# Optimization experiments

Measured on AMD Instinct MI355X. Metric: run time of the kernel, lower is better.

Reference implementation:

```python
import jax, jax.numpy as jnp
import numpy as np

B, S, D = 4, 2048, 2048
E = 8            # num_experts
TOP_K = 2
H = 1408         # intermediate_size per expert
SH = 2 * H       # shared expert intermediate (shared_experts=2)


def setup_inputs() -> dict:
    key = jax.random.key(0)
    ks = jax.random.split(key, 8)
    sc = 0.02
    return {
        "hidden_states": jax.random.normal(ks[0], (B, S, D), jnp.float32),
        "gate_w": jax.random.normal(ks[1], (E, D), jnp.float32) * sc,   # torch Linear weight [out,in]
        "w1": jax.random.normal(ks[2], (E, H, D), jnp.float32) * sc,    # gate_proj per expert
        "w3": jax.random.normal(ks[3], (E, H, D), jnp.float32) * sc,    # up_proj per expert
        "w2": jax.random.normal(ks[4], (E, D, H), jnp.float32) * sc,    # down_proj per expert
        "sw1": jax.random.normal(ks[5], (SH, D), jnp.float32) * sc,
        "sw3": jax.random.normal(ks[6], (SH, D), jnp.float32) * sc,
        "sw2": jax.random.normal(ks[7], (D, SH), jnp.float32) * sc,
    }


def reference(hidden_states, gate_w, w1, w3, w2, sw1, sw3, sw2):
    b, s, d = hidden_states.shape
    x = hidden_states.reshape(-1, d)                      # [T, D]
    logits = x @ gate_w.T                                 # [T, E]
    rw, sel = jax.lax.top_k(logits, TOP_K)                # [T, K]
    rw = jax.nn.softmax(rw, axis=-1)                      # norm_topk_prob=True
    onehot = jax.nn.one_hot(sel, E, dtype=x.dtype)        # [T, K, E]
    token_mask = onehot.sum(axis=1)                       # [T, E] in {0,1}
    # NOTE: faithful to the source quirk: expert_weights.sum(dim=-1) on a flat
    # masked gather sums routing weights over ALL tokens selecting the expert,
    # producing one scalar per expert.
    s_e = (rw[..., None] * onehot).sum(axis=(0, 1))       # [E]
    combine = token_mask * s_e                            # [T, E]
    # per-expert SwiGLU MLP on all tokens (dense combine form of gather/scatter)
    g = jnp.einsum('td,ehd->eth', x, w1)                  # [E, T, H]
    u = jnp.einsum('td,ehd->eth', x, w3)
    a = jax.nn.silu(g) * u
    y = jnp.einsum('eth,edh->etd', a, w2)                 # [E, T, D]
    out = jnp.einsum('te,etd->td', combine, y)            # [T, D]
    shared = (jax.nn.silu(x @ sw1.T) * (x @ sw3.T)) @ sw2.T
    out = out + shared
    return out.reshape(b, s, d)
```

## Files before the change

kernel.cpp:

```cpp
#include <hip/hip_runtime.h>
#include <hip/hip_bf16.h>
#include <stdint.h>

#define T_TOK 8192
#define DIM   2048
#define NEXP  8
#define HDIM  1408
#define SHDIM 2816

typedef __attribute__((ext_vector_type(8))) short bfrag;
typedef __attribute__((ext_vector_type(4))) float f32x4;
typedef __attribute__((ext_vector_type(4))) short s16x4;

__device__ __forceinline__ short f2bf(float f) {
    union { float f; uint32_t u; } v; v.f = f;
    return (short)((v.u + 0x8000u) >> 16);
}
__device__ __forceinline__ float bf2f(short s) {
    union { uint32_t u; float f; } v; v.u = ((uint32_t)(uint16_t)s) << 16;
    return v.f;
}

__device__ __forceinline__ bfrag cvt8(float4 a, float4 b) {
    bfrag r;
    r[0] = f2bf(a.x); r[1] = f2bf(a.y); r[2] = f2bf(a.z); r[3] = f2bf(a.w);
    r[4] = f2bf(b.x); r[5] = f2bf(b.y); r[6] = f2bf(b.z); r[7] = f2bf(b.w);
    return r;
}

__device__ __forceinline__ void gload16(const void* g, void* l) {
    __builtin_amdgcn_global_load_lds(
        (__attribute__((address_space(1))) void*)(g),
        (__attribute__((address_space(3))) void*)(l), 16, 0, 0);
}

#define MFMA16(a, b, c) __builtin_amdgcn_mfma_f32_16x16x32_bf16((a), (b), (c), 0, 0, 0)


__global__ __launch_bounds__(256) void gate_kernel(
    const float* __restrict__ x, const float* __restrict__ gw,
    __hip_bfloat16* __restrict__ xbf,
    int* __restrict__ sel, int* __restrict__ meta, float* __restrict__ s_e)
{
    __shared__ float g[NEXP * DIM];
    for (int i = threadIdx.x; i < NEXP * DIM; i += 256) g[i] = gw[i];
    __syncthreads();
    const int wid = threadIdx.x >> 6, lane = threadIdx.x & 63;
    for (int it = 0; it < 8; ++it) {
        const int t = blockIdx.x * 32 + wid * 8 + it;
        float acc[NEXP];
#pragma unroll
        for (int e = 0; e < NEXP; ++e) acc[e] = 0.f;
        const float4* xr = (const float4*)(x + (size_t)t * DIM);
        for (int j = 0; j < DIM / 4; j += 64) {
            float4 xv = xr[j + lane];
            s16x4 xv16 = { f2bf(xv.x), f2bf(xv.y), f2bf(xv.z), f2bf(xv.w) };
            *(s16x4*)&xbf[(size_t)t * DIM + (j + lane) * 4] = xv16;
#pragma unroll
            for (int e = 0; e < NEXP; ++e) {
                float4 gv = *(const float4*)&g[e * DIM + (j + lane) * 4];
                acc[e] += xv.x * gv.x + xv.y * gv.y + xv.z * gv.z + xv.w * gv.w;
            }
        }
#pragma unroll
        for (int e = 0; e < NEXP; ++e)
            for (int o = 32; o; o >>= 1) acc[e] += __shfl_xor(acc[e], o);
        if (lane == 0) {
            int e0 = 0; float v0 = acc[0];
#pragma unroll
            for (int e = 1; e < NEXP; ++e) if (acc[e] > v0) { v0 = acc[e]; e0 = e; }
            int e1 = -1; float v1 = -3.4e38f;
#pragma unroll
            for (int e = 0; e < NEXP; ++e) if (e != e0 && acc[e] > v1) { v1 = acc[e]; e1 = e; }
            float p0 = 1.f / (1.f + __expf(v1 - v0));
            float p1 = 1.f - p0;
            sel[2 * t] = e0; sel[2 * t + 1] = e1;
            atomicAdd(&s_e[e0], p0); atomicAdd(&s_e[e1], p1);
            atomicAdd(&meta[e0], 1); atomicAdd(&meta[e1], 1);
        }
    }
}

__global__ void scan_kernel(int* meta) {
    if (threadIdx.x == 0) {
        int acc = 0;
        for (int e = 0; e < NEXP; ++e) {
            meta[16 + e] = acc;
            meta[8 + e]  = acc;
            acc += meta[e];
        }
        meta[24] = acc;
    }
}

__global__ __launch_bounds__(256) void fill_kernel(
    const int* __restrict__ sel, int* __restrict__ meta,
    int* __restrict__ list, int2* __restrict__ slots)
{
    const int t = blockIdx.x * 256 + threadIdx.x;
    int e0 = sel[2 * t], e1 = sel[2 * t + 1];
    int p0 = atomicAdd(&meta[8 + e0], 1); list[p0] = t;
    int p1 = atomicAdd(&meta[8 + e1], 1); list[p1] = t;
    slots[t] = make_int2(p0, p1);
}

#define C1 2883584
#define C2 5767168
#define C3 8650752
#define C4 9371648
#define C5 10092544
#define C6 10813440
__global__ __launch_bounds__(256) void cvt6_kernel(
    const float* __restrict__ s0, const float* __restrict__ s1, const float* __restrict__ s2,
    const float* __restrict__ s3, const float* __restrict__ s4, const float* __restrict__ s5,
    __hip_bfloat16* __restrict__ d0, __hip_bfloat16* __restrict__ d1, __hip_bfloat16* __restrict__ d2,
    __hip_bfloat16* __restrict__ d3, __hip_bfloat16* __restrict__ d4, __hip_bfloat16* __restrict__ d5)
{
    const int stride = gridDim.x * 256;
    for (int i = blockIdx.x * 256 + threadIdx.x; i < C6; i += stride) {
        const float* s; __hip_bfloat16* d; int off;
        if      (i < C1) { s = s0; d = d0; off = i; }
        else if (i < C2) { s = s1; d = d1; off = i - C1; }
        else if (i < C3) { s = s2; d = d2; off = i - C2; }
        else if (i < C4) { s = s3; d = d3; off = i - C3; }
        else if (i < C5) { s = s4; d = d4; off = i - C4; }
        else             { s = s5; d = d5; off = i - C5; }
        const float4* p = (const float4*)(s + (size_t)off * 8);
        float4 a = p[0], b = p[1];
        *(bfrag*)(d + (size_t)off * 8) = cvt8(a, b);
    }
}


template<int N, bool GATHER>
__global__ __launch_bounds__(512, 2) void up_v6(
    const __hip_bfloat16* __restrict__ X,
    const __hip_bfloat16* __restrict__ W1,
    const __hip_bfloat16* __restrict__ W3,
    __hip_bfloat16* __restrict__ act,
    const int* __restrict__ list,
    const int* __restrict__ meta)
{
    constexpr int K = DIM;
    constexpr int NP = K / 32;
    constexpr int nx = N / 128, ny = T_TOK / 256, nz = GATHER ? NEXP : 1;
    constexpr int nwg = nx * ny * nz, cpx = nwg / 8;
    const int bid = (int)blockIdx.x + nx * ((int)blockIdx.y + ny * (int)blockIdx.z);
    const int virt = (bid & 7) * cpx + (bid >> 3);
    const int xi = virt % nx;
    const int rest = virt / nx;
    const int yi = rest % ny;
    const int e = rest / ny;

    int count, base;
    if (GATHER) {
        count = meta[e]; base = meta[16 + e];
        if (yi * 256 >= count) return;
    } else { count = T_TOK; base = 0; }
    const int m0 = yi * 256, n0 = xi * 128;

    __shared__ alignas(16) short As[4][256 * 32];
    __shared__ alignas(16) short B1s[4][128 * 32];
    __shared__ alignas(16) short B3s[4][128 * 32];

    const int tid = threadIdx.x, wid = tid >> 6, lane = tid & 63;

    const int u    = (tid & 7) ^ ((tid >> 3) & 7);
    const int srow = 2 * (tid >> 3) + (u >> 2);
    const int sslot = u & 3;

    const __hip_bfloat16* pA[2];
#pragma unroll
    for (int q = 0; q < 2; ++q) {
        int r = m0 + srow + q * 128; if (r > count - 1) r = count - 1;
        int ga = GATHER ? list[base + r] : r;
        pA[q] = X + (size_t)ga * K + sslot * 8;
    }
    const __hip_bfloat16* pB1 = W1 + ((size_t)e * N + n0 + srow) * K + sslot * 8;
    const __hip_bfloat16* pB3 = W3 + ((size_t)e * N + n0 + srow) * K + sslot * 8;

#define STAGE_UP(H, BUF) do { const int k0_ = (H) * 32;                         \
    gload16(pA[0] + k0_, &As[BUF][tid * 8]);                                    \
    gload16(pA[1] + k0_, &As[BUF][4096 + tid * 8]);                             \
    gload16(pB1   + k0_, &B1s[BUF][tid * 8]);                                   \
    gload16(pB3   + k0_, &B3s[BUF][tid * 8]); } while (0)

    const int wm = wid >> 2, wn = wid & 3;
    const int l15 = lane & 15, lhi = lane >> 4;
    const int vswz = (((lhi + 4 * (l15 & 1)) ^ (l15 >> 1)) << 4);
    const int arb  = (l15 >> 1) * 128 + vswz;

    f32x4 accg[8][2], accu[8][2];
#pragma unroll
    for (int i = 0; i < 8; ++i)
#pragma unroll
        for (int j = 0; j < 2; ++j) { accg[i][j] = 0.f; accu[i][j] = 0.f; }

    STAGE_UP(0, 0);
    STAGE_UP(1, 1);
    STAGE_UP(2, 2);

#pragma unroll 4
    for (int p = 0; p < NP; ++p) {
        const int cur = p & 3;
        asm volatile("s_waitcnt vmcnt(8)" ::: "memory");
        __builtin_amdgcn_s_barrier();
        __builtin_amdgcn_sched_barrier(0);
        const int ps = (p + 3 < NP) ? (p + 3) : (NP - 1);
        STAGE_UP(ps, (p + 3) & 3);
        __builtin_amdgcn_sched_barrier(0);
        bfrag b1f[2], b3f[2];
#pragma unroll
        for (int j = 0; j < 2; ++j) {
            const int off = wn * 2048 + j * 1024 + arb;
            b1f[j] = *(const bfrag*)((const char*)B1s[cur] + off);
            b3f[j] = *(const bfrag*)((const char*)B3s[cur] + off);
        }
        __builtin_amdgcn_s_setprio(1);
#pragma unroll
        for (int i = 0; i < 8; ++i) {
            bfrag a = *(const bfrag*)((const char*)As[cur] + wm * 8192 + i * 1024 + arb);
#pragma unroll
            for (int j = 0; j < 2; ++j) {
                accg[i][j] = MFMA16(a, b1f[j], accg[i][j]);
                accu[i][j] = MFMA16(a, b3f[j], accu[i][j]);
            }
        }
        __builtin_amdgcn_s_setprio(0);
    }
#undef STAGE_UP
    asm volatile("s_waitcnt vmcnt(0)" ::: "memory");

#pragma unroll
    for (int i = 0; i < 8; ++i)
#pragma unroll
        for (int r = 0; r < 4; ++r) {
            int m = wm * 128 + i * 16 + lhi * 4 + r;
            if (m0 + m < count) {
#pragma unroll
                for (int j = 0; j < 2; ++j) {
                    float gg = accg[i][j][r];
                    float uu = accu[i][j][r];
                    float a = gg / (1.f + __expf(-gg)) * uu;
                    int n = n0 + wn * 32 + j * 16 + l15;
                    act[(size_t)(base + m0 + m) * N + n] = __float2bfloat16(a);
                }
            }
        }
}

template<int KD, bool TO_BF16>
__global__ __launch_bounds__(512, 2) void down_v6(
    const __hip_bfloat16* __restrict__ A,
    const __hip_bfloat16* __restrict__ W2,
    float* __restrict__ out,
    __hip_bfloat16* __restrict__ yscr,
    const int* __restrict__ meta)
{
    constexpr int N = DIM;
    constexpr int NP = KD / 32;
    constexpr int nx = N / 256, ny = T_TOK / 256, nz = TO_BF16 ? NEXP : 1;
    constexpr int nwg = nx * ny * nz, cpx = nwg / 8;
    const int bid = (int)blockIdx.x + nx * ((int)blockIdx.y + ny * (int)blockIdx.z);
    const int virt = (bid & 7) * cpx + (bid >> 3);
    const int xi = virt % nx;
    const int rest = virt / nx;
    const int yi = rest % ny;
    const int e = rest / ny;

    int count, base;
    if (TO_BF16) {
        count = meta[e]; base = meta[16 + e];
        if (yi * 256 >= count) return;
    } else { count = T_TOK; base = 0; }
    const int m0 = yi * 256, n0 = xi * 256;

    __shared__ alignas(16) short As[4][256 * 32];
    __shared__ alignas(16) short Bs[4][256 * 32];

    const int tid = threadIdx.x, wid = tid >> 6, lane = tid & 63;

    const int u    = (tid & 7) ^ ((tid >> 3) & 7);
    const int srow = 2 * (tid >> 3) + (u >> 2);
    const int sslot = u & 3;

    const __hip_bfloat16* pA[2];
    const __hip_bfloat16* pB[2];
#pragma unroll
    for (int q = 0; q < 2; ++q) {
        int r = m0 + srow + q * 128; if (r > count - 1) r = count - 1;
        pA[q] = A  + (size_t)(base + r) * KD + sslot * 8;
        pB[q] = W2 + ((size_t)e * N + n0 + srow + q * 128) * KD + sslot * 8;
    }

#define STAGE_DN(H, BUF) do { const int k0_ = (H) * 32;                         \
    gload16(pA[0] + k0_, &As[BUF][tid * 8]);                                    \
    gload16(pA[1] + k0_, &As[BUF][4096 + tid * 8]);                             \
    gload16(pB[0] + k0_, &Bs[BUF][tid * 8]);                                    \
    gload16(pB[1] + k0_, &Bs[BUF][4096 + tid * 8]); } while (0)

    const int wm = wid >> 2, wn = wid & 3;
    const int l15 = lane & 15, lhi = lane >> 4;
    const int vswz = (((lhi + 4 * (l15 & 1)) ^ (l15 >> 1)) << 4);
    const int arb  = (l15 >> 1) * 128 + vswz;

    f32x4 acc[8][4];
#pragma unroll
    for (int i = 0; i < 8; ++i)
#pragma unroll
        for (int j = 0; j < 4; ++j) acc[i][j] = 0.f;

    STAGE_DN(0, 0);
    STAGE_DN(1, 1);
    STAGE_DN(2, 2);

#pragma unroll 4
    for (int p = 0; p < NP; ++p) {
        const int cur = p & 3;
        asm volatile("s_waitcnt vmcnt(8)" ::: "memory");
        __builtin_amdgcn_s_barrier();
        __builtin_amdgcn_sched_barrier(0);
        const int ps = (p + 3 < NP) ? (p + 3) : (NP - 1);
        STAGE_DN(ps, (p + 3) & 3);
        __builtin_amdgcn_sched_barrier(0);
        bfrag bf[4];
#pragma unroll
        for (int j = 0; j < 4; ++j)
            bf[j] = *(const bfrag*)((const char*)Bs[cur] + wn * 4096 + j * 1024 + arb);
        __builtin_amdgcn_s_setprio(1);
#pragma unroll
        for (int i = 0; i < 8; ++i) {
            bfrag a = *(const bfrag*)((const char*)As[cur] + wm * 8192 + i * 1024 + arb);
#pragma unroll
            for (int j = 0; j < 4; ++j)
                acc[i][j] = MFMA16(a, bf[j], acc[i][j]);
        }
        __builtin_amdgcn_s_setprio(0);
    }
#undef STAGE_DN
    asm volatile("s_waitcnt vmcnt(0)" ::: "memory");

#pragma unroll
    for (int i = 0; i < 8; ++i)
#pragma unroll
        for (int r = 0; r < 4; ++r) {
            int m = wm * 128 + i * 16 + lhi * 4 + r;
            if (m0 + m < count) {
#pragma unroll
                for (int j = 0; j < 4; ++j) {
                    int n = n0 + wn * 64 + j * 16 + l15;
                    if (TO_BF16)
                        yscr[(size_t)(base + m0 + m) * DIM + n] = __float2bfloat16(acc[i][j][r]);
                    else
                        out[(size_t)(m0 + m) * DIM + n] = acc[i][j][r];
                }
            }
        }
}

__global__ __launch_bounds__(256) void combine_kernel(
    float* __restrict__ out, const __hip_bfloat16* __restrict__ yscr,
    const int* __restrict__ sel, const int2* __restrict__ slots,
    const float* __restrict__ s_e)
{
    const int t = blockIdx.x;
    const int d = threadIdx.x * 8;
    const int2 sl = slots[t];
    const float se0 = s_e[sel[2 * t]];
    const float se1 = s_e[sel[2 * t + 1]];
    bfrag y0 = *(const bfrag*)&yscr[(size_t)sl.x * DIM + d];
    bfrag y1 = *(const bfrag*)&yscr[(size_t)sl.y * DIM + d];
    float4* o = (float4*)(out + (size_t)t * DIM + d);
    float4 o0 = o[0], o1 = o[1];
    o0.x += se0 * bf2f(y0[0]) + se1 * bf2f(y1[0]);
    o0.y += se0 * bf2f(y0[1]) + se1 * bf2f(y1[1]);
    o0.z += se0 * bf2f(y0[2]) + se1 * bf2f(y1[2]);
    o0.w += se0 * bf2f(y0[3]) + se1 * bf2f(y1[3]);
    o1.x += se0 * bf2f(y0[4]) + se1 * bf2f(y1[4]);
    o1.y += se0 * bf2f(y0[5]) + se1 * bf2f(y1[5]);
    o1.z += se0 * bf2f(y0[6]) + se1 * bf2f(y1[6]);
    o1.w += se0 * bf2f(y0[7]) + se1 * bf2f(y1[7]);
    o[0] = o0; o[1] = o1;
}

extern "C" void kernel_launch(void* const* d_in, const int* in_sizes, int n_in,
                              void* d_out, int out_size, void* d_ws, size_t ws_size,
                              hipStream_t stream) {
    const float* x   = (const float*)d_in[0];
    const float* gw  = (const float*)d_in[1];
    const float* w1  = (const float*)d_in[2];
    const float* w3  = (const float*)d_in[3];
    const float* w2  = (const float*)d_in[4];
    const float* sw1 = (const float*)d_in[5];
    const float* sw3 = (const float*)d_in[6];
    const float* sw2 = (const float*)d_in[7];
    float* out = (float*)d_out;

    const size_t SZ_X   = (size_t)T_TOK * DIM * 2;
    const size_t SZ_W   = (size_t)NEXP * HDIM * DIM * 2;
    const size_t SZ_SW  = (size_t)SHDIM * DIM * 2;
    const size_t SZ_ACT = (size_t)2 * T_TOK * HDIM * 2;
    const size_t need = SZ_X + 3 * SZ_W + 3 * SZ_SW + SZ_ACT
                      + (size_t)4 * T_TOK * sizeof(int)
                      + (size_t)2 * T_TOK * sizeof(int)  + 512;
    if (need > ws_size) return;

    char* p = (char*)d_ws;
    __hip_bfloat16* xbf   = (__hip_bfloat16*)p; p += SZ_X;
    __hip_bfloat16* w1bf  = (__hip_bfloat16*)p; p += SZ_W;
    __hip_bfloat16* w3bf  = (__hip_bfloat16*)p; p += SZ_W;
    __hip_bfloat16* w2bf  = (__hip_bfloat16*)p; p += SZ_W;
    __hip_bfloat16* sw1bf = (__hip_bfloat16*)p; p += SZ_SW;
    __hip_bfloat16* sw3bf = (__hip_bfloat16*)p; p += SZ_SW;
    __hip_bfloat16* sw2bf = (__hip_bfloat16*)p; p += SZ_SW;
    __hip_bfloat16* act   = (__hip_bfloat16*)p; p += SZ_ACT;
    int*  list  = (int*)p;  p += (size_t)2 * T_TOK * sizeof(int);
    int*  sel   = (int*)p;  p += (size_t)2 * T_TOK * sizeof(int);
    int2* slots = (int2*)p; p += (size_t)2 * T_TOK * sizeof(int);
    int*  meta  = (int*)p;
    float* s_e  = (float*)(meta + 32);
    __hip_bfloat16* yscr = (__hip_bfloat16*)d_ws;

    hipMemsetAsync(meta, 0, 256, stream);
    gate_kernel<<<T_TOK / 32, 256, 0, stream>>>(x, gw, xbf, sel, meta, s_e);
    scan_kernel<<<1, 64, 0, stream>>>(meta);
    fill_kernel<<<T_TOK / 256, 256, 0, stream>>>(sel, meta, list, slots);

    cvt6_kernel<<<2048, 256, 0, stream>>>(w1, w3, w2, sw1, sw3, sw2,
                                          w1bf, w3bf, w2bf, sw1bf, sw3bf, sw2bf);

    up_v6<SHDIM, false><<<dim3(SHDIM / 128, T_TOK / 256, 1), 512, 0, stream>>>(
        xbf, sw1bf, sw3bf, act, nullptr, meta);
    down_v6<SHDIM, false><<<dim3(DIM / 256, T_TOK / 256, 1), 512, 0, stream>>>(
        act, sw2bf, out, nullptr, meta);
    up_v6<HDIM, true><<<dim3(HDIM / 128, T_TOK / 256, NEXP), 512, 0, stream>>>(
        xbf, w1bf, w3bf, act, list, meta);
    down_v6<HDIM, true><<<dim3(DIM / 256, T_TOK / 256, NEXP), 512, 0, stream>>>(
        act, w2bf, out, yscr, meta);
    combine_kernel<<<T_TOK, 256, 0, stream>>>(out, yscr, sel, slots, s_e);
}
```

Baseline: 1.118 ms.

## Split GEMM k-step into two barrier-separated phases interleaving loads with MFMA

Each k-iteration of the up and down GEMM kernels is split into two halves. The A-tile global-to-LDS loads are issued before the first half of the MFMAs and the B-tile loads before the second half. Fragment reads are hoisted ahead of explicit lgkmcnt fences and workgroup barriers, in a ping-pong style schedule. The aim is to spread memory issue across the MFMA work and keep the waves in lockstep, at the cost of four extra barriers per iteration.

```diff
diff --git a/kernel.cpp b/kernel.cpp
--- a/kernel.cpp
+++ b/kernel.cpp
@@ -35,6 +35,8 @@
 }
 
 #define MFMA16(a, b, c) __builtin_amdgcn_mfma_f32_16x16x32_bf16((a), (b), (c), 0, 0, 0)
+#define LGKM0_FENCE() do { asm volatile("s_waitcnt lgkmcnt(0)" ::: "memory"); \
+                           __builtin_amdgcn_sched_barrier(0); } while (0)
 
 
 __global__ __launch_bounds__(256) void gate_kernel(
@@ -133,7 +135,7 @@
 
 
 template<int N, bool GATHER>
-__global__ __launch_bounds__(512, 2) void up_v6(
+__global__ __launch_bounds__(512, 2) void up_v7(
     const __hip_bfloat16* __restrict__ X,
     const __hip_bfloat16* __restrict__ W1,
     const __hip_bfloat16* __restrict__ W3,
@@ -179,56 +181,84 @@
     const __hip_bfloat16* pB1 = W1 + ((size_t)e * N + n0 + srow) * K + sslot * 8;
     const __hip_bfloat16* pB3 = W3 + ((size_t)e * N + n0 + srow) * K + sslot * 8;
 
-#define STAGE_UP(H, BUF) do { const int k0_ = (H) * 32;                         \
+    const int wm = wid >> 2, wn = wid & 3;
+    const int l15 = lane & 15, lhi = lane >> 4;
+    const int vswz = (((lhi + 4 * (l15 & 1)) ^ (l15 >> 1)) << 4);
+    const int arb  = (l15 >> 1) * 128 + vswz;
+
+    f32x4 accg[8][2], accu[8][2];
+#pragma unroll
+    for (int i = 0; i < 8; ++i)
+#pragma unroll
+        for (int j = 0; j < 2; ++j) { accg[i][j] = 0.f; accu[i][j] = 0.f; }
+
+#define STAGE_ALL(H, BUF) do { const int k0_ = (H) * 32;                        \
     gload16(pA[0] + k0_, &As[BUF][tid * 8]);                                    \
     gload16(pA[1] + k0_, &As[BUF][4096 + tid * 8]);                             \
     gload16(pB1   + k0_, &B1s[BUF][tid * 8]);                                   \
     gload16(pB3   + k0_, &B3s[BUF][tid * 8]); } while (0)
-
-    const int wm = wid >> 2, wn = wid & 3;
-    const int l15 = lane & 15, lhi = lane >> 4;
-    const int vswz = (((lhi + 4 * (l15 & 1)) ^ (l15 >> 1)) << 4);
-    const int arb  = (l15 >> 1) * 128 + vswz;
-
-    f32x4 accg[8][2], accu[8][2];
-#pragma unroll
-    for (int i = 0; i < 8; ++i)
-#pragma unroll
-        for (int j = 0; j < 2; ++j) { accg[i][j] = 0.f; accu[i][j] = 0.f; }
-
-    STAGE_UP(0, 0);
-    STAGE_UP(1, 1);
-    STAGE_UP(2, 2);
+    STAGE_ALL(0, 0);
+    STAGE_ALL(1, 1);
+    STAGE_ALL(2, 2);
+#undef STAGE_ALL
 
 #pragma unroll 4
     for (int p = 0; p < NP; ++p) {
         const int cur = p & 3;
+        const int ps = (p + 3 < NP) ? (p + 3) : (NP - 1);
+        const int pb = (p + 3) & 3;
+        const int k0s = ps * 32;
+
         asm volatile("s_waitcnt vmcnt(8)" ::: "memory");
         __builtin_amdgcn_s_barrier();
         __builtin_amdgcn_sched_barrier(0);
-        const int ps = (p + 3 < NP) ? (p + 3) : (NP - 1);
-        STAGE_UP(ps, (p + 3) & 3);
-        __builtin_amdgcn_sched_barrier(0);
-        bfrag b1f[2], b3f[2];
+        gload16(pA[0] + k0s, &As[pb][tid * 8]);
+        gload16(pA[1] + k0s, &As[pb][4096 + tid * 8]);
+        __builtin_amdgcn_sched_barrier(0);
+        bfrag b1f[2], b3f[2], af[4];
 #pragma unroll
         for (int j = 0; j < 2; ++j) {
             const int off = wn * 2048 + j * 1024 + arb;
             b1f[j] = *(const bfrag*)((const char*)B1s[cur] + off);
             b3f[j] = *(const bfrag*)((const char*)B3s[cur] + off);
         }
+#pragma unroll
+        for (int i = 0; i < 4; ++i)
+            af[i] = *(const bfrag*)((const char*)As[cur] + wm * 8192 + i * 1024 + arb);
+        __builtin_amdgcn_s_barrier();
+        LGKM0_FENCE();
         __builtin_amdgcn_s_setprio(1);
 #pragma unroll
-        for (int i = 0; i < 8; ++i) {
-            bfrag a = *(const bfrag*)((const char*)As[cur] + wm * 8192 + i * 1024 + arb);
+        for (int i = 0; i < 4; ++i)
 #pragma unroll
             for (int j = 0; j < 2; ++j) {
-                accg[i][j] = MFMA16(a, b1f[j], accg[i][j]);
-                accu[i][j] = MFMA16(a, b3f[j], accu[i][j]);
+                accg[i][j] = MFMA16(af[i], b1f[j], accg[i][j]);
+                accu[i][j] = MFMA16(af[i], b3f[j], accu[i][j]);
             }
-        }
         __builtin_amdgcn_s_setprio(0);
-    }
-#undef STAGE_UP
+        __builtin_amdgcn_s_barrier();
+
+        __builtin_amdgcn_sched_barrier(0);
+        gload16(pB1 + k0s, &B1s[pb][tid * 8]);
+        gload16(pB3 + k0s, &B3s[pb][tid * 8]);
+        __builtin_amdgcn_sched_barrier(0);
+        bfrag ag[4];
+#pragma unroll
+        for (int i = 0; i < 4; ++i)
+            ag[i] = *(const bfrag*)((const char*)As[cur] + wm * 8192 + (4 + i) * 1024 + arb);
+        __builtin_amdgcn_s_barrier();
+        LGKM0_FENCE();
+        __builtin_amdgcn_s_setprio(1);
+#pragma unroll
+        for (int i = 0; i < 4; ++i)
+#pragma unroll
+            for (int j = 0; j < 2; ++j) {
+                accg[4 + i][j] = MFMA16(ag[i], b1f[j], accg[4 + i][j]);
+                accu[4 + i][j] = MFMA16(ag[i], b3f[j], accu[4 + i][j]);
+            }
+        __builtin_amdgcn_s_setprio(0);
+        __builtin_amdgcn_s_barrier();
+    }
     asm volatile("s_waitcnt vmcnt(0)" ::: "memory");
 
 #pragma unroll
@@ -250,7 +280,7 @@
 }
 
 template<int KD, bool TO_BF16>
-__global__ __launch_bounds__(512, 2) void down_v6(
+__global__ __launch_bounds__(512, 2) void down_v7(
     const __hip_bfloat16* __restrict__ A,
     const __hip_bfloat16* __restrict__ W2,
     float* __restrict__ out,
@@ -293,51 +323,77 @@
         pB[q] = W2 + ((size_t)e * N + n0 + srow + q * 128) * KD + sslot * 8;
     }
 
-#define STAGE_DN(H, BUF) do { const int k0_ = (H) * 32;                         \
+    const int wm = wid >> 2, wn = wid & 3;
+    const int l15 = lane & 15, lhi = lane >> 4;
+    const int vswz = (((lhi + 4 * (l15 & 1)) ^ (l15 >> 1)) << 4);
+    const int arb  = (l15 >> 1) * 128 + vswz;
+
+    f32x4 acc[8][4];
+#pragma unroll
+    for (int i = 0; i < 8; ++i)
+#pragma unroll
+        for (int j = 0; j < 4; ++j) acc[i][j] = 0.f;
+
+#define STAGE_ALL(H, BUF) do { const int k0_ = (H) * 32;                        \
     gload16(pA[0] + k0_, &As[BUF][tid * 8]);                                    \
     gload16(pA[1] + k0_, &As[BUF][4096 + tid * 8]);                             \
     gload16(pB[0] + k0_, &Bs[BUF][tid * 8]);                                    \
     gload16(pB[1] + k0_, &Bs[BUF][4096 + tid * 8]); } while (0)
-
-    const int wm = wid >> 2, wn = wid & 3;
-    const int l15 = lane & 15, lhi = lane >> 4;
-    const int vswz = (((lhi + 4 * (l15 & 1)) ^ (l15 >> 1)) << 4);
-    const int arb  = (l15 >> 1) * 128 + vswz;
-
-    f32x4 acc[8][4];
-#pragma unroll
-    for (int i = 0; i < 8; ++i)
-#pragma unroll
-        for (int j = 0; j < 4; ++j) acc[i][j] = 0.f;
-
-    STAGE_DN(0, 0);
-    STAGE_DN(1, 1);
-    STAGE_DN(2, 2);
+    STAGE_ALL(0, 0);
+    STAGE_ALL(1, 1);
+    STAGE_ALL(2, 2);
+#undef STAGE_ALL
 
 #pragma unroll 4
     for (int p = 0; p < NP; ++p) {
         const int cur = p & 3;
+        const int ps = (p + 3 < NP) ? (p + 3) : (NP - 1);
+        const int pb = (p + 3) & 3;
+        const int k0s = ps * 32;
+
         asm volatile("s_waitcnt vmcnt(8)" ::: "memory");
         __builtin_amdgcn_s_barrier();
         __builtin_amdgcn_sched_barrier(0);
-        const int ps = (p + 3 < NP) ? (p + 3) : (NP - 1);
-        STAGE_DN(ps, (p + 3) & 3);
-        __builtin_amdgcn_sched_barrier(0);
-        bfrag bf[4];
+        gload16(pA[0] + k0s, &As[pb][tid * 8]);
+        gload16(pA[1] + k0s, &As[pb][4096 + tid * 8]);
+        __builtin_amdgcn_sched_barrier(0);
+        bfrag bf[4], af[4];
 #pragma unroll
         for (int j = 0; j < 4; ++j)
             bf[j] = *(const bfrag*)((const char*)Bs[cur] + wn * 4096 + j * 1024 + arb);
+#pragma unroll
+        for (int i = 0; i < 4; ++i)
+            af[i] = *(const bfrag*)((const char*)As[cur] + wm * 8192 + i * 1024 + arb);
+        __builtin_amdgcn_s_barrier();
+        LGKM0_FENCE();
         __builtin_amdgcn_s_setprio(1);
 #pragma unroll
-        for (int i = 0; i < 8; ++i) {
-            bfrag a = *(const bfrag*)((const char*)As[cur] + wm * 8192 + i * 1024 + arb);
+        for (int i = 0; i < 4; ++i)
 #pragma unroll
             for (int j = 0; j < 4; ++j)
-                acc[i][j] = MFMA16(a, bf[j], acc[i][j]);
-        }
+                acc[i][j] = MFMA16(af[i], bf[j], acc[i][j]);
         __builtin_amdgcn_s_setprio(0);
-    }
-#undef STAGE_DN
+        __builtin_amdgcn_s_barrier();
+
+        __builtin_amdgcn_sched_barrier(0);
+        gload16(pB[0] + k0s, &Bs[pb][tid * 8]);
+        gload16(pB[1] + k0s, &Bs[pb][4096 + tid * 8]);
+        __builtin_amdgcn_sched_barrier(0);
+        bfrag ag[4];
+#pragma unroll
+        for (int i = 0; i < 4; ++i)
+            ag[i] = *(const bfrag*)((const char*)As[cur] + wm * 8192 + (4 + i) * 1024 + arb);
+        __builtin_amdgcn_s_barrier();
+        LGKM0_FENCE();
+        __builtin_amdgcn_s_setprio(1);
+#pragma unroll
+        for (int i = 0; i < 4; ++i)
+#pragma unroll
+            for (int j = 0; j < 4; ++j)
+                acc[4 + i][j] = MFMA16(ag[i], bf[j], acc[4 + i][j]);
+        __builtin_amdgcn_s_setprio(0);
+        __builtin_amdgcn_s_barrier();
+    }
     asm volatile("s_waitcnt vmcnt(0)" ::: "memory");
 
 #pragma unroll
@@ -429,13 +485,13 @@
     cvt6_kernel<<<2048, 256, 0, stream>>>(w1, w3, w2, sw1, sw3, sw2,
                                           w1bf, w3bf, w2bf, sw1bf, sw3bf, sw2bf);
 
-    up_v6<SHDIM, false><<<dim3(SHDIM / 128, T_TOK / 256, 1), 512, 0, stream>>>(
+    up_v7<SHDIM, false><<<dim3(SHDIM / 128, T_TOK / 256, 1), 512, 0, stream>>>(
         xbf, sw1bf, sw3bf, act, nullptr, meta);
-    down_v6<SHDIM, false><<<dim3(DIM / 256, T_TOK / 256, 1), 512, 0, stream>>>(
+    down_v7<SHDIM, false><<<dim3(DIM / 256, T_TOK / 256, 1), 512, 0, stream>>>(
         act, sw2bf, out, nullptr, meta);
-    up_v6<HDIM, true><<<dim3(HDIM / 128, T_TOK / 256, NEXP), 512, 0, stream>>>(
+    up_v7<HDIM, true><<<dim3(HDIM / 128, T_TOK / 256, NEXP), 512, 0, stream>>>(
         xbf, w1bf, w3bf, act, list, meta);
-    down_v6<HDIM, true><<<dim3(DIM / 256, T_TOK / 256, NEXP), 512, 0, stream>>>(
+    down_v7<HDIM, true><<<dim3(DIM / 256, T_TOK / 256, NEXP), 512, 0, stream>>>(
         act, w2bf, out, yscr, meta);
     combine_kernel<<<T_TOK, 256, 0, stream>>>(out, yscr, sel, slots, s_e);
 }
```

Result: no change. 1.105 ms (-1.2%).
